# Kernel tuning notes

Hardware: AMD Instinct MI355X
Metric: run time of the kernel (lower is better)

The kernel has to match this reference:

```python
import jax, jax.numpy as jnp
import numpy as np

T, B, D = 512, 16, 512
H, DH, DI, L = 8, 64, 2048, 4
EPS = 1e-6
SCALE = 1.0 / DH ** 0.5
NEG_INF = -1e9


def _ln(x, g, b):
    m = jnp.mean(x, axis=-1, keepdims=True)
    v = jnp.var(x, axis=-1, keepdims=True)
    return (x - m) * jax.lax.rsqrt(v + EPS) * g + b


def _pos_emb(pos_seq):
    inv_freq = 1.0 / (10000.0 ** (jnp.arange(0, D, 2, dtype=jnp.float32) / D))
    s = pos_seq[:, None] * inv_freq[None, :]  # (rlen, D/2)
    return jnp.concatenate([jnp.sin(s), jnp.cos(s)], axis=-1)  # (rlen, D)


def _rel_shift(x, klen):
    # faithful reshape-slice trick: (q, r, b, n) -> view as (r, q, b, n), drop first, back to (q, r-1, b, n)
    q, r, b, n = x.shape
    x = x.reshape(r, q, b, n)[1:].reshape(q, r - 1, b, n)
    return x[:, :klen]


def _layer(h, r, r_w_bias, r_r_bias, attn_mask, qkv_w, r_net_w, o_w,
           ln1_g, ln1_b, w1, b1, w2, b2, ln2_g, ln2_b):
    qlen, bsz, _ = h.shape
    rlen = r.shape[0]
    w_heads = jnp.einsum('ibd,de->ibe', h, qkv_w)
    q, k, v = jnp.split(w_heads, 3, axis=-1)
    q = q.reshape(qlen, bsz, H, DH)
    k = k.reshape(qlen, bsz, H, DH)
    v = v.reshape(qlen, bsz, H, DH)
    rk = jnp.einsum('jbd,de->jbe', r, r_net_w).reshape(rlen, bsz, H, DH)
    AC = jnp.einsum('ibnd,jbnd->ijbn', q + r_w_bias, k)
    BD = _rel_shift(jnp.einsum('ibnd,jbnd->ijbn', q + r_r_bias, rk), qlen)
    score = (AC + BD) * SCALE
    score = jnp.where(attn_mask[None, :, :, None], NEG_INF, score)
    prob = jax.nn.softmax(score, axis=1)
    vec = jnp.einsum('ijbn,jbnd->ibnd', prob, v).reshape(qlen, bsz, H * DH)
    out = _ln(h + jnp.einsum('ibe,ed->ibd', vec, o_w), ln1_g, ln1_b)
    ff = jnp.maximum(jnp.einsum('ibd,df->ibf', out, w1) + b1, 0.0)
    ff = jnp.einsum('ibf,fd->ibd', ff, w2) + b2
    return _ln(out + ff, ln2_g, ln2_b)


def setup_inputs() -> dict:
    key = jax.random.key(0)
    ks = jax.random.split(key, 12)
    s = 0.02
    lengths = jax.random.randint(ks[0], (B,), T // 2, T + 1)
    seq_mask = jnp.arange(T)[None, :] < lengths[:, None]  # (B, T) bool, True = real token
    return {
        'h': jax.random.normal(ks[1], (B, T, D), jnp.float32),
        'seq_mask': seq_mask,
        'r_w_bias': jax.random.normal(ks[2], (H, DH), jnp.float32) * s,
        'r_r_bias': jax.random.normal(ks[3], (H, DH), jnp.float32) * s,
        'top_ln_g': jnp.ones((D,), jnp.float32),
        'top_ln_b': jnp.zeros((D,), jnp.float32),
        'qkv_w': jax.random.normal(ks[4], (L, D, 3 * H * DH), jnp.float32) * s,
        'r_net_w': jax.random.normal(ks[5], (L, D, H * DH), jnp.float32) * s,
        'o_w': jax.random.normal(ks[6], (L, H * DH, D), jnp.float32) * s,
        'attn_ln_g': jnp.ones((L, D), jnp.float32),
        'attn_ln_b': jnp.zeros((L, D), jnp.float32),
        'ff_w1': jax.random.normal(ks[7], (L, D, DI), jnp.float32) * s,
        'ff_b1': jnp.zeros((L, DI), jnp.float32),
        'ff_w2': jax.random.normal(ks[8], (L, DI, D), jnp.float32) * s,
        'ff_b2': jnp.zeros((L, D), jnp.float32),
        'ff_ln_g': jnp.ones((L, D), jnp.float32),
        'ff_ln_b': jnp.zeros((L, D), jnp.float32),
    }


def reference(h, seq_mask, r_w_bias, r_r_bias, top_ln_g, top_ln_b, qkv_w, r_net_w, o_w,
              attn_ln_g, attn_ln_b, ff_w1, ff_b1, ff_w2, ff_b2, ff_ln_g, ff_ln_b):
    h = jnp.transpose(h, (1, 0, 2))            # (T, B, D)
    attn_mask = ~jnp.transpose(seq_mask, (1, 0))  # (T, B), True = padding
    fw = _pos_emb(jnp.arange(T, -T, -1, dtype=h.dtype))
    bw = _pos_emb(jnp.arange(-T, T, 1, dtype=h.dtype))
    pos = jnp.concatenate([
        jnp.broadcast_to(fw[:, None, :], (2 * T, B // 2, D)),
        jnp.broadcast_to(bw[:, None, :], (2 * T, B - B // 2, D)),
    ], axis=1)                                 # (2T, B, D)
    h = _ln(h, top_ln_g, top_ln_b)
    hids = [h]
    out = h
    for i in range(L):
        out = _layer(out, pos, r_w_bias, r_r_bias, attn_mask,
                     qkv_w[i], r_net_w[i], o_w[i], attn_ln_g[i], attn_ln_b[i],
                     ff_w1[i], ff_b1[i], ff_w2[i], ff_b2[i], ff_ln_g[i], ff_ln_b[i])
        hids.append(out)
    out = jnp.transpose(out, (1, 0, 2))
    hids = tuple(jnp.transpose(x, (1, 0, 2)) for x in hids)
    return (out, hids)
```

## Files before the change

kernel.cpp:

```cpp
#include <hip/hip_runtime.h>
#include <cstddef>


typedef unsigned short u16;
typedef short s16x8 __attribute__((ext_vector_type(8)));
typedef unsigned short u16x8 __attribute__((ext_vector_type(8)));
typedef float f32x4 __attribute__((ext_vector_type(4)));

__device__ __forceinline__ u16 f2bf(float f) {
  unsigned int u = __float_as_uint(f);
  u += 0x7fffu + ((u >> 16) & 1u);
  return (u16)(u >> 16);
}
__device__ __forceinline__ float bf2f(u16 u) {
  return __uint_as_float((unsigned int)u << 16);
}

__device__ __forceinline__ f32x4 mfma16(s16x8 a, s16x8 b, f32x4 c) {
  return __builtin_amdgcn_mfma_f32_16x16x32_bf16(a, b, c, 0, 0, 0);
}

__device__ __forceinline__ void gl2lds16(const u16* g, u16* l) {
  __builtin_amdgcn_global_load_lds(
      (const __attribute__((address_space(1))) unsigned int*)g,
      (__attribute__((address_space(3))) unsigned int*)l, 16, 0, 0);
}

template <int MODE, int TN>
__launch_bounds__(256) __global__
void gemm_bt(const u16* __restrict__ A, const u16* __restrict__ Bt,
             int M, int N, int K,
             void* p0, void* p1, void* p2, void* p3,
             const float* __restrict__ p4, const float* __restrict__ p5) {
  (void)M;
  constexpr int NT = TN / 32;
  constexpr int NBQ = TN / 32;
  __shared__ u16 As[128 * 64];
  __shared__ u16 Bs[TN * 64];
  const int tid = threadIdx.x;
  const int lane = tid & 63;
  const int w = tid >> 6;
  const int quad = lane >> 4, l15 = lane & 15;
  const int m0 = blockIdx.y << 7, n0 = blockIdx.x * TN;

  if constexpr (MODE == 0) {
    const int lz = blockIdx.z >> 1, gz = blockIdx.z & 1;
    A += (size_t)gz * 524288;
    Bt += (size_t)lz * 262144;
    p0 = (void*)((u16*)p0 + (size_t)lz * 1048576 + (size_t)gz * 524288);
  }

  f32x4 acc[4][NT];
#pragma unroll
  for (int a = 0; a < 4; ++a)
#pragma unroll
    for (int b = 0; b < NT; ++b) {
      f32x4 z = {0.f, 0.f, 0.f, 0.f};
      acc[a][b] = z;
    }

  const int rg = lane >> 3;
  const int cz = ((lane & 7) ^ rg) << 3;
  const u16* gA = A + (size_t)(m0 + w * 8 + rg) * K + cz;
  const u16* gB = Bt + (size_t)(n0 + w * 8 + rg) * K + cz;
  u16* lA = &As[w * 512];
  u16* lB = &Bs[w * 512];

  const int wm = (w >> 1) << 6, wn = (w & 1) * (NT * 16);
  const int rsw = l15 & 7;
  const int nk = K >> 6;
  for (int kt = 0; kt < nk; ++kt) {
    const int k0 = kt << 6;
#pragma unroll
    for (int q = 0; q < 4; ++q)
      gl2lds16(gA + (size_t)(q * 32) * K + k0, lA + q * 2048);
#pragma unroll
    for (int q = 0; q < NBQ; ++q)
      gl2lds16(gB + (size_t)(q * 32) * K + k0, lB + q * 2048);
    __syncthreads();
#pragma unroll
    for (int ks = 0; ks < 2; ++ks) {
      const int co = ((ks * 4 + quad) ^ rsw) << 3;
      s16x8 af[4], bfg[NT];
#pragma unroll
      for (int t = 0; t < 4; ++t)
        af[t] = *(const s16x8*)&As[(wm + t * 16 + l15) * 64 + co];
#pragma unroll
      for (int t = 0; t < NT; ++t)
        bfg[t] = *(const s16x8*)&Bs[(wn + t * 16 + l15) * 64 + co];
#pragma unroll
      for (int mt = 0; mt < 4; ++mt)
#pragma unroll
        for (int nt = 0; nt < NT; ++nt)
          acc[mt][nt] = mfma16(af[mt], bfg[nt], acc[mt][nt]);
    }
    __syncthreads();
  }

#pragma unroll
  for (int mt = 0; mt < 4; ++mt) {
#pragma unroll
    for (int nt = 0; nt < NT; ++nt) {
#pragma unroll
      for (int r = 0; r < 4; ++r) {
        const int row = m0 + wm + mt * 16 + quad * 4 + r;
        const int col = n0 + wn + nt * 16 + l15;
        const float v = acc[mt][nt][r];
        if constexpr (MODE == 0) {
          const int hn = col >> 6, d = col & 63;
          ((u16*)p0)[((size_t)hn * 1024 + row) * 64 + d] = f2bf(v);
        } else if constexpr (MODE == 1) {
          const int i = row >> 4, b = row & 15;
          const int which = col >> 9, hn = (col >> 6) & 7, d = col & 63;
          const int bn = b * 8 + hn;
          const size_t idx = ((size_t)bn * 512 + i) * 64 + d;
          if (which == 0) {
            ((u16*)p0)[idx] = f2bf(v + p4[hn * 64 + d]);
            ((u16*)p1)[idx] = f2bf(v + p5[hn * 64 + d]);
          } else if (which == 1) {
            ((u16*)p2)[idx] = f2bf(v);
          } else {
            ((u16*)p3)[idx] = f2bf(v);
          }
        } else if constexpr (MODE == 2) {
          ((float*)p0)[(size_t)row * N + col] =
              v + ((const float*)p1)[(size_t)row * N + col];
        } else if constexpr (MODE == 3) {
          ((float*)p0)[(size_t)row * N + col] =
              v + ((const float*)p1)[(size_t)row * N + col] +
              ((const float*)p2)[col];
        } else {
          float t = v + ((const float*)p1)[col];
          ((u16*)p0)[(size_t)row * N + col] = f2bf(t > 0.f ? t : 0.f);
        }
      }
    }
  }
}

__launch_bounds__(256) __global__
void transpose_w_kernel(const float* __restrict__ qkv, const float* __restrict__ rnet,
                        const float* __restrict__ ow, const float* __restrict__ w1,
                        const float* __restrict__ w2, u16* __restrict__ dst) {
  const int type = blockIdx.z, l = blockIdx.y, tile = blockIdx.x;
  int R, C;
  const float* src;
  u16* out;
  switch (type) {
    case 0: R = 512; C = 1536; src = qkv + (size_t)l * 786432; out = dst + (size_t)l * 786432; break;
    case 1: R = 512; C = 512;  src = rnet + (size_t)l * 262144; out = dst + 3145728 + (size_t)l * 262144; break;
    case 2: R = 512; C = 512;  src = ow + (size_t)l * 262144;   out = dst + 4194304 + (size_t)l * 262144; break;
    case 3: R = 512; C = 2048; src = w1 + (size_t)l * 1048576;  out = dst + 5242880 + (size_t)l * 1048576; break;
    default: R = 2048; C = 512; src = w2 + (size_t)l * 1048576; out = dst + 9437184 + (size_t)l * 1048576; break;
  }
  const int tC = C >> 6;
  const int tR = R >> 6;
  if (tile >= tC * tR) return;
  const int r0 = (tile / tC) << 6, c0 = (tile % tC) << 6;
  __shared__ float tb[64][65];
  const int tid = threadIdx.x;
  const int rr = tid >> 2, cc = (tid & 3) << 4;
#pragma unroll
  for (int j = 0; j < 4; ++j) {
    f32x4 u = *(const f32x4*)(src + (size_t)(r0 + rr) * C + c0 + cc + j * 4);
    tb[rr][cc + j * 4 + 0] = u[0];
    tb[rr][cc + j * 4 + 1] = u[1];
    tb[rr][cc + j * 4 + 2] = u[2];
    tb[rr][cc + j * 4 + 3] = u[3];
  }
  __syncthreads();
  u16x8 o0, o1;
#pragma unroll
  for (int j = 0; j < 8; ++j) o0[j] = f2bf(tb[cc + j][rr]);
#pragma unroll
  for (int j = 0; j < 8; ++j) o1[j] = f2bf(tb[cc + 8 + j][rr]);
  *(u16x8*)(out + (size_t)(c0 + rr) * R + r0 + cc) = o0;
  *(u16x8*)(out + (size_t)(c0 + rr) * R + r0 + cc + 8) = o1;
}

__launch_bounds__(256) __global__
void posemb_kernel(u16* __restrict__ r_bf) {
  const int idx = blockIdx.x * 256 + threadIdx.x;
  const int d = idx & 511, j = (idx >> 9) & 1023, g = idx >> 19;
  const float pos = g ? (float)(j - 512) : (float)(512 - j);
  const int dp = d & 255;
  const float invf = expf((float)dp * (-9.210340371976184f / 256.f));
  const float v = pos * invf;
  r_bf[idx] = f2bf((d < 256) ? sinf(v) : cosf(v));
}

__launch_bounds__(256) __global__
void transpose_v_kernel(const u16* __restrict__ Vb, u16* __restrict__ Vt) {
  const int bn = blockIdx.y, j0 = blockIdx.x << 6;
  __shared__ u16 tb[64][72];
  const int tid = threadIdx.x;
#pragma unroll
  for (int q = 0; q < 2; ++q) {
    const int s = q * 256 + tid;
    const int jj = s >> 3, c = s & 7;
    u16x8 u = *(const u16x8*)(Vb + ((size_t)bn * 512 + j0 + jj) * 64 + c * 8);
    *(u16x8*)&tb[jj][c * 8] = u;
  }
  __syncthreads();
#pragma unroll
  for (int q = 0; q < 2; ++q) {
    const int s = q * 256 + tid;
    const int d = s >> 3, c = s & 7;
    u16x8 o;
#pragma unroll
    for (int e = 0; e < 8; ++e) o[e] = tb[c * 8 + e][d];
    *(u16x8*)(Vt + ((size_t)bn * 64 + d) * 512 + j0 + c * 8) = o;
  }
}

#define ATTN_FENCE_BAR()                                    \
  do {                                                      \
    asm volatile("s_waitcnt lgkmcnt(0)" ::: "memory");      \
    __builtin_amdgcn_s_barrier();                           \
    __builtin_amdgcn_sched_barrier(0);                      \
  } while (0)

__launch_bounds__(256) __global__
void attn_kernel(const u16* __restrict__ Qw, const u16* __restrict__ Qr,
                 const u16* __restrict__ Kb, const u16* __restrict__ Vt,
                 const u16* __restrict__ rkb, const int* __restrict__ smask,
                 u16* __restrict__ vecb) {
  __shared__ u16 Ks[4096];
  __shared__ u16 Vts[4096];
  __shared__ u16 Band[8192];
  __shared__ u16 Ps[4096];

  const int tid = threadIdx.x, lane = tid & 63, w = tid >> 6;
  const int quad = lane >> 4, l15 = lane & 15;
  const int bn = blockIdx.x, b = bn >> 3, n = bn & 7;
  const int g = (b >= 8) ? 1 : 0;
  const int i0 = blockIdx.y << 6;

  unsigned mbits = 0;
  const int* smb = smask + b * 512 + l15;
#pragma unroll
  for (int s = 0; s < 32; ++s)
    if (smb[s * 16]) mbits |= 1u << s;
  unsigned vmask = 0;
#pragma unroll
  for (int jt = 0; jt < 8; ++jt)
    if (__any((int)((mbits >> (jt * 4)) & 15u))) vmask |= 1u << jt;
  const int ntiles = vmask ? (32 - __clz((int)vmask)) : 0;

  const u16* qwp = Qw + ((size_t)bn * 512 + i0 + w * 16 + l15) * 64 + quad * 8;
  const u16* qrp = Qr + ((size_t)bn * 512 + i0 + w * 16 + l15) * 64 + quad * 8;
  const s16x8 qw0 = *(const s16x8*)qwp, qw1 = *(const s16x8*)(qwp + 32);
  const s16x8 qr0 = *(const s16x8*)qrp, qr1 = *(const s16x8*)(qrp + 32);

  const u16* kbase = Kb + (size_t)bn * (512 * 64);
  const u16* vbase = Vt + (size_t)bn * (64 * 512);
  const u16* rkg = rkb + (size_t)(g * 8 + n) * (1024 * 64);

  const int s0 = w * 64 + lane;
  const int rl = s0 >> 3;
  const int cd = ((s0 & 7) ^ (rl & 7)) * 8;
  u16* lK0 = &Ks[w * 512];
  u16* lK1 = &Ks[(4 + w) * 512];
  u16* lV0 = &Vts[w * 512];
  u16* lV1 = &Vts[(4 + w) * 512];
  u16* lBq[4] = {&Band[w * 512], &Band[(4 + w) * 512], &Band[(8 + w) * 512],
                 &Band[(12 + w) * 512]};
  u16* pwv = &Ps[w * 1024];

  const int sw8 = ((quad ^ (l15 & 7)) * 8);
  const int sw8b = (((quad ^ (l15 & 7)) ^ 4) * 8);

  int sl[4], hisel[4];
#pragma unroll
  for (int r = 0; r < 4; ++r) {
    const int e = 15 + l15 - quad * 4 - r;
    sl[r] = (quad << 4) | (e & 15);
    hisel[r] = e >> 4;
  }

  f32x4 O[4];
  float m_st[4], l_st[4];
#pragma unroll
  for (int t = 0; t < 4; ++t) {
    f32x4 z = {0.f, 0.f, 0.f, 0.f};
    O[t] = z;
    m_st[t] = -1e30f;
    l_st[t] = 0.f;
  }

  s16x8 rK0, rK1, rV0, rV1, rB0, rB1;
  auto issue_prefetch = [&](int nt) {
    const int j0n = nt << 6;
    const int jr0n = 449 + j0n - i0;
    rK0 = *(const s16x8*)(kbase + (size_t)(j0n + rl) * 64 + cd);
    rK1 = *(const s16x8*)(kbase + (size_t)(j0n + 32 + rl) * 64 + cd);
    rV0 = *(const s16x8*)(vbase + (size_t)rl * 512 + j0n + cd);
    rV1 = *(const s16x8*)(vbase + (size_t)(rl + 32) * 512 + j0n + cd);
    int rr0 = jr0n + 64 + rl;
    int rr1 = jr0n + 96 + rl;
    rr0 = rr0 < 1023 ? rr0 : 1023;
    rr1 = rr1 < 1023 ? rr1 : 1023;
    rB0 = *(const s16x8*)(rkg + (size_t)rr0 * 64 + cd);
    rB1 = *(const s16x8*)(rkg + (size_t)rr1 * 64 + cd);
  };

  for (int jt = 0; jt < ntiles; ++jt) {
    if (jt == 0) {
      const int jr00 = 449 - i0;
      gl2lds16(kbase + (size_t)rl * 64 + cd, lK0);
      gl2lds16(kbase + (size_t)(32 + rl) * 64 + cd, lK1);
      gl2lds16(vbase + (size_t)rl * 512 + cd, lV0);
      gl2lds16(vbase + (size_t)(rl + 32) * 512 + cd, lV1);
#pragma unroll
      for (int q = 0; q < 4; ++q) {
        int rrow = jr00 + q * 32 + rl;
        rrow = rrow < 1023 ? rrow : 1023;
        gl2lds16(rkg + (size_t)rrow * 64 + cd, lBq[q]);
      }
      asm volatile("" ::: "memory");
      __builtin_amdgcn_sched_barrier(0);
      if (ntiles > 1) {
        issue_prefetch(1);
        asm volatile("s_waitcnt vmcnt(6)" ::: "memory");
      } else {
        asm volatile("s_waitcnt vmcnt(0)" ::: "memory");
      }
      __builtin_amdgcn_s_barrier();
      __builtin_amdgcn_sched_barrier(0);
    } else {
      ATTN_FENCE_BAR();
      *(s16x8*)(lK0 + lane * 8) = rK0;
      *(s16x8*)(lK1 + lane * 8) = rK1;
      *(s16x8*)(lV0 + lane * 8) = rV0;
      *(s16x8*)(lV1 + lane * 8) = rV1;
      const int segb = ((jt + 1) & 1) << 1;
      *(s16x8*)(lBq[segb] + lane * 8) = rB0;
      *(s16x8*)(lBq[segb + 1] + lane * 8) = rB1;
      if (jt + 1 < ntiles) issue_prefetch(jt + 1);
      ATTN_FENCE_BAR();
    }

    f32x4 ac[4];
#pragma unroll
    for (int t = 0; t < 4; ++t) {
      f32x4 z = {0.f, 0.f, 0.f, 0.f};
      ac[t] = z;
      s16x8 k0f = *(const s16x8*)&Ks[(t * 16 + l15) * 64 + sw8];
      s16x8 k1f = *(const s16x8*)&Ks[(t * 16 + l15) * 64 + sw8b];
      ac[t] = mfma16(qw0, k0f, ac[t]);
      ac[t] = mfma16(qw1, k1f, ac[t]);
    }
    const int bb0 = 48 - w * 16;
    const int rofs = (jt & 1) << 6;
    f32x4 bd[5];
#pragma unroll
    for (int t = 0; t < 5; ++t) {
      f32x4 z = {0.f, 0.f, 0.f, 0.f};
      const int prow = ((bb0 + t * 16 + l15) + rofs) & 127;
      s16x8 b0f = *(const s16x8*)&Band[prow * 64 + sw8];
      s16x8 b1f = *(const s16x8*)&Band[prow * 64 + sw8b];
      bd[t] = mfma16(qr1, b1f, mfma16(qr0, b0f, z));
    }
    float sh[5][4];
#pragma unroll
    for (int t = 0; t < 5; ++t)
#pragma unroll
      for (int r = 0; r < 4; ++r) sh[t][r] = __shfl(bd[t][r], sl[r]);

    float pv[4][4];
#pragma unroll
    for (int t = 0; t < 4; ++t) {
      const float mk = ((mbits >> (jt * 4 + t)) & 1u) ? 0.f : -1e9f;
#pragma unroll
      for (int r = 0; r < 4; ++r) {
        const float bdv = hisel[r] ? sh[t + 1][r] : sh[t][r];
        pv[t][r] = (ac[t][r] + bdv) * 0.125f + mk;
      }
    }
#pragma unroll
    for (int r = 0; r < 4; ++r) {
      float mx = fmaxf(fmaxf(pv[0][r], pv[1][r]), fmaxf(pv[2][r], pv[3][r]));
#pragma unroll
      for (int xm = 1; xm < 16; xm <<= 1) mx = fmaxf(mx, __shfl_xor(mx, xm));
      const float mn = fmaxf(m_st[r], mx);
      const float al = __expf(m_st[r] - mn);
      m_st[r] = mn;
      float rs = 0.f;
#pragma unroll
      for (int t = 0; t < 4; ++t) {
        pv[t][r] = __expf(pv[t][r] - mn);
        rs += pv[t][r];
      }
#pragma unroll
      for (int xm = 1; xm < 16; xm <<= 1) rs += __shfl_xor(rs, xm);
      l_st[r] = l_st[r] * al + rs;
#pragma unroll
      for (int t = 0; t < 4; ++t) O[t][r] *= al;
    }
#pragma unroll
    for (int t = 0; t < 4; ++t)
#pragma unroll
      for (int r = 0; r < 4; ++r) {
        const int row = quad * 4 + r, col = t * 16 + l15;
        pwv[row * 64 + ((((col >> 3) ^ row) & 7) << 3) + (col & 7)] =
            f2bf(pv[t][r]);
      }
#pragma unroll
    for (int ks = 0; ks < 2; ++ks) {
      const int ch = (((ks * 4 + quad) ^ l15) & 7) << 3;
      s16x8 pf = *(const s16x8*)&pwv[l15 * 64 + ch];
#pragma unroll
      for (int td = 0; td < 4; ++td) {
        s16x8 vf = *(const s16x8*)&Vts[(td * 16 + l15) * 64 +
                                       (ks == 0 ? sw8 : sw8b)];
        O[td] = mfma16(pf, vf, O[td]);
      }
    }
  }

#pragma unroll
  for (int td = 0; td < 4; ++td) {
#pragma unroll
    for (int r = 0; r < 4; ++r) {
      const int i = i0 + w * 16 + quad * 4 + r;
      const float val = O[td][r] / l_st[r];
      vecb[((size_t)i * 16 + b) * 512 + n * 64 + td * 16 + l15] = f2bf(val);
    }
  }
}

__launch_bounds__(256) __global__
void ln_kernel(const float* __restrict__ src, int src_is_bt,
               const float* __restrict__ gw, const float* __restrict__ bww,
               float* __restrict__ dst32, u16* __restrict__ dstbf,
               float* __restrict__ o1, float* __restrict__ o2) {
  const int row = blockIdx.x * 4 + (threadIdx.x >> 6);
  const int lane = threadIdx.x & 63;
  const int i = row >> 4, b = row & 15;
  const float* x = src + (src_is_bt ? ((size_t)b * 512 + i) * 512 : (size_t)row * 512);
  f32x4 u0 = *(const f32x4*)(x + lane * 8);
  f32x4 u1 = *(const f32x4*)(x + lane * 8 + 4);
  float s = u0[0] + u0[1] + u0[2] + u0[3] + u1[0] + u1[1] + u1[2] + u1[3];
  float sq = u0[0] * u0[0] + u0[1] * u0[1] + u0[2] * u0[2] + u0[3] * u0[3] +
             u1[0] * u1[0] + u1[1] * u1[1] + u1[2] * u1[2] + u1[3] * u1[3];
  for (int m = 1; m < 64; m <<= 1) {
    s += __shfl_xor(s, m);
    sq += __shfl_xor(sq, m);
  }
  const float mean = s * (1.f / 512.f);
  const float var = sq * (1.f / 512.f) - mean * mean;
  const float rs = rsqrtf(var + 1e-6f);
  f32x4 g0 = *(const f32x4*)(gw + lane * 8);
  f32x4 g1 = *(const f32x4*)(gw + lane * 8 + 4);
  f32x4 b0 = *(const f32x4*)(bww + lane * 8);
  f32x4 b1 = *(const f32x4*)(bww + lane * 8 + 4);
  f32x4 y0, y1;
#pragma unroll
  for (int k = 0; k < 4; ++k) {
    y0[k] = (u0[k] - mean) * rs * g0[k] + b0[k];
    y1[k] = (u1[k] - mean) * rs * g1[k] + b1[k];
  }
  const size_t o_ib = (size_t)row * 512 + lane * 8;
  const size_t o_tb = ((size_t)b * 512 + i) * 512 + lane * 8;
  if (dst32) {
    *(f32x4*)(dst32 + o_ib) = y0;
    *(f32x4*)(dst32 + o_ib + 4) = y1;
  }
  if (dstbf) {
    u16x8 ov;
#pragma unroll
    for (int k = 0; k < 4; ++k) {
      ov[k] = f2bf(y0[k]);
      ov[k + 4] = f2bf(y1[k]);
    }
    *(u16x8*)(dstbf + o_ib) = ov;
  }
  if (o1) {
    *(f32x4*)(o1 + o_tb) = y0;
    *(f32x4*)(o1 + o_tb + 4) = y1;
  }
  if (o2) {
    *(f32x4*)(o2 + o_tb) = y0;
    *(f32x4*)(o2 + o_tb + 4) = y1;
  }
}

extern "C" void kernel_launch(void* const* d_in, const int* in_sizes, int n_in,
                              void* d_out, int out_size, void* d_ws, size_t ws_size,
                              hipStream_t stream) {
  (void)in_sizes; (void)n_in; (void)out_size; (void)ws_size;
  const float* h_in = (const float*)d_in[0];
  const int* smask = (const int*)d_in[1];
  const float* rwb = (const float*)d_in[2];
  const float* rrb = (const float*)d_in[3];
  const float* top_g = (const float*)d_in[4];
  const float* top_b = (const float*)d_in[5];
  const float* qkv_w = (const float*)d_in[6];
  const float* rnet_w = (const float*)d_in[7];
  const float* o_w = (const float*)d_in[8];
  const float* attn_g = (const float*)d_in[9];
  const float* attn_b = (const float*)d_in[10];
  const float* w1 = (const float*)d_in[11];
  const float* b1 = (const float*)d_in[12];
  const float* w2 = (const float*)d_in[13];
  const float* b2 = (const float*)d_in[14];
  const float* ff_g = (const float*)d_in[15];
  const float* ff_b = (const float*)d_in[16];
  float* out = (float*)d_out;
  const size_t BTD = 4194304;

  char* ws = (char*)d_ws;
  size_t off = 0;
  auto alloc = [&](size_t bytes) {
    void* p = ws + off;
    off += (bytes + 255) & ~(size_t)255;
    return p;
  };
  u16* wT = (u16*)alloc(13631488ull * 2);
  u16* r_bf = (u16*)alloc(2ull * 1024 * 512 * 2);
  u16* rkb = (u16*)alloc(8ull << 20);
  u16* Qw = (u16*)alloc(8ull << 20);
  u16* Qr = (u16*)alloc(8ull << 20);
  u16* Kb = (u16*)alloc(8ull << 20);
  u16* Vt = (u16*)alloc(8ull << 20);
  u16* vecb = (u16*)alloc(8ull << 20);
  u16* Xbf = (u16*)alloc(8ull << 20);
  u16* ffbf = (u16*)alloc(32ull << 20);
  float* hcur = (float*)alloc(16ull << 20);
  float* tmp = (float*)Qw;
  float* mid = (float*)Kb;
  u16* Vb = ffbf;

  dim3 blk(256);
  transpose_w_kernel<<<dim3(256, 4, 5), blk, 0, stream>>>(qkv_w, rnet_w, o_w, w1, w2, wT);
  posemb_kernel<<<dim3(4096), blk, 0, stream>>>(r_bf);
  ln_kernel<<<dim3(2048), blk, 0, stream>>>(h_in, 1, top_g, top_b, hcur, Xbf,
                                            out + BTD, (float*)nullptr);

  gemm_bt<0, 64><<<dim3(8, 8, 8), blk, 0, stream>>>(
      r_bf, wT + 3145728, 1024, 512, 512,
      rkb, nullptr, nullptr, nullptr, nullptr, nullptr);

  for (int l = 0; l < 4; ++l) {
    u16* qkvT = wT + (size_t)l * 786432;
    u16* oT = wT + 4194304 + (size_t)l * 262144;
    u16* w1T = wT + 5242880 + (size_t)l * 1048576;
    u16* w2T = wT + 9437184 + (size_t)l * 1048576;

    gemm_bt<1, 128><<<dim3(12, 64), blk, 0, stream>>>(
        Xbf, qkvT, 8192, 1536, 512, Qw, Qr, Kb, Vb, rwb, rrb);

    transpose_v_kernel<<<dim3(8, 128), blk, 0, stream>>>(Vb, Vt);

    attn_kernel<<<dim3(128, 8), blk, 0, stream>>>(
        Qw, Qr, Kb, Vt, rkb + (size_t)l * 1048576, smask, vecb);

    gemm_bt<2, 64><<<dim3(8, 64), blk, 0, stream>>>(
        vecb, oT, 8192, 512, 512, tmp, hcur, nullptr, nullptr, nullptr, nullptr);

    ln_kernel<<<dim3(2048), blk, 0, stream>>>(tmp, 0, attn_g + l * 512, attn_b + l * 512,
                                              mid, Xbf, (float*)nullptr, (float*)nullptr);

    gemm_bt<4, 128><<<dim3(16, 64), blk, 0, stream>>>(
        Xbf, w1T, 8192, 2048, 512, ffbf, (void*)(b1 + (size_t)l * 2048),
        nullptr, nullptr, nullptr, nullptr);

    gemm_bt<3, 64><<<dim3(8, 64), blk, 0, stream>>>(
        ffbf, w2T, 8192, 512, 2048, tmp, mid, (void*)(b2 + (size_t)l * 512),
        nullptr, nullptr, nullptr);

    ln_kernel<<<dim3(2048), blk, 0, stream>>>(
        tmp, 0, ff_g + l * 512, ff_b + l * 512, hcur, Xbf,
        out + (size_t)(2 + l) * BTD, (l == 3) ? out : (float*)nullptr);
  }
}
```

Baseline: 1.016 ms.

## Software-pipeline GEMM K-loop with register prefetch of next tile

The GEMM main loop now loads the next K tile from global memory into registers while the current tile is computed from LDS. The registers are then written to LDS between two barriers, replacing the old pattern of direct global-to-LDS loads followed by a full sync each iteration. The goal is to hide global memory latency behind the MFMA work. In exchange it costs more registers, which may lower occupancy, and it relies on hand-written vmcnt wait counts. The attention fence macro is renamed and shared with the GEMM.

```diff
diff --git a/kernel.cpp b/kernel.cpp
--- a/kernel.cpp
+++ b/kernel.cpp
@@ -25,6 +25,13 @@
       (const __attribute__((address_space(1))) unsigned int*)g,
       (__attribute__((address_space(3))) unsigned int*)l, 16, 0, 0);
 }
+
+#define FENCE_BAR()                                         \
+  do {                                                      \
+    asm volatile("s_waitcnt lgkmcnt(0)" ::: "memory");      \
+    __builtin_amdgcn_s_barrier();                           \
+    __builtin_amdgcn_sched_barrier(0);                      \
+  } while (0)
 
 template <int MODE, int TN>
 __launch_bounds__(256) __global__
@@ -35,7 +42,7 @@
   (void)M;
   constexpr int NT = TN / 32;
   constexpr int NBQ = TN / 32;
-  __shared__ u16 As[128 * 64];
+  __shared__ u16 As[8192];
   __shared__ u16 Bs[TN * 64];
   const int tid = threadIdx.x;
   const int lane = tid & 63;
@@ -69,15 +76,50 @@
   const int wm = (w >> 1) << 6, wn = (w & 1) * (NT * 16);
   const int rsw = l15 & 7;
   const int nk = K >> 6;
+
+  s16x8 pA[4], pB[NBQ];
+  auto prefetch = [&](int kt) {
+    const int k0 = kt << 6;
+#pragma unroll
+    for (int q = 0; q < 4; ++q)
+      pA[q] = *(const s16x8*)(gA + (size_t)(q * 32) * K + k0);
+#pragma unroll
+    for (int q = 0; q < NBQ; ++q)
+      pB[q] = *(const s16x8*)(gB + (size_t)(q * 32) * K + k0);
+  };
+
+#pragma unroll
+  for (int q = 0; q < 4; ++q)
+    gl2lds16(gA + (size_t)(q * 32) * K, lA + q * 2048);
+#pragma unroll
+  for (int q = 0; q < NBQ; ++q)
+    gl2lds16(gB + (size_t)(q * 32) * K, lB + q * 2048);
+  asm volatile("" ::: "memory");
+  __builtin_amdgcn_sched_barrier(0);
+  if (nk > 1) {
+    prefetch(1);
+    if constexpr (NBQ == 4)
+      asm volatile("s_waitcnt vmcnt(8)" ::: "memory");
+    else
+      asm volatile("s_waitcnt vmcnt(6)" ::: "memory");
+  } else {
+    asm volatile("s_waitcnt vmcnt(0)" ::: "memory");
+  }
+  __builtin_amdgcn_s_barrier();
+  __builtin_amdgcn_sched_barrier(0);
+
   for (int kt = 0; kt < nk; ++kt) {
-    const int k0 = kt << 6;
-#pragma unroll
-    for (int q = 0; q < 4; ++q)
-      gl2lds16(gA + (size_t)(q * 32) * K + k0, lA + q * 2048);
-#pragma unroll
-    for (int q = 0; q < NBQ; ++q)
-      gl2lds16(gB + (size_t)(q * 32) * K + k0, lB + q * 2048);
-    __syncthreads();
+    if (kt > 0) {
+      FENCE_BAR();
+#pragma unroll
+      for (int q = 0; q < 4; ++q)
+        *(s16x8*)(lA + q * 2048 + lane * 8) = pA[q];
+#pragma unroll
+      for (int q = 0; q < NBQ; ++q)
+        *(s16x8*)(lB + q * 2048 + lane * 8) = pB[q];
+      if (kt + 1 < nk) prefetch(kt + 1);
+      FENCE_BAR();
+    }
 #pragma unroll
     for (int ks = 0; ks < 2; ++ks) {
       const int co = ((ks * 4 + quad) ^ rsw) << 3;
@@ -94,7 +136,6 @@
         for (int nt = 0; nt < NT; ++nt)
           acc[mt][nt] = mfma16(af[mt], bfg[nt], acc[mt][nt]);
     }
-    __syncthreads();
   }
 
 #pragma unroll
@@ -213,13 +254,6 @@
   }
 }
 
-#define ATTN_FENCE_BAR()                                    \
-  do {                                                      \
-    asm volatile("s_waitcnt lgkmcnt(0)" ::: "memory");      \
-    __builtin_amdgcn_s_barrier();                           \
-    __builtin_amdgcn_sched_barrier(0);                      \
-  } while (0)
-
 __launch_bounds__(256) __global__
 void attn_kernel(const u16* __restrict__ Qw, const u16* __restrict__ Qr,
                  const u16* __restrict__ Kb, const u16* __restrict__ Vt,
@@ -328,7 +362,7 @@
       __builtin_amdgcn_s_barrier();
       __builtin_amdgcn_sched_barrier(0);
     } else {
-      ATTN_FENCE_BAR();
+      FENCE_BAR();
       *(s16x8*)(lK0 + lane * 8) = rK0;
       *(s16x8*)(lK1 + lane * 8) = rK1;
       *(s16x8*)(lV0 + lane * 8) = rV0;
@@ -337,7 +371,7 @@
       *(s16x8*)(lBq[segb] + lane * 8) = rB0;
       *(s16x8*)(lBq[segb + 1] + lane * 8) = rB1;
       if (jt + 1 < ntiles) issue_prefetch(jt + 1);
-      ATTN_FENCE_BAR();
+      FENCE_BAR();
     }
 
     f32x4 ac[4];
```

Result: faster. 993.1 us (-2.2%).
